# Kernel tuning notes

Hardware: AMD Instinct MI355X
Metric: run time of the kernel (lower is better)

## Reference

```python
import jax, jax.numpy as jnp
import numpy as np

K = 16          # neighbors per center (init arg K)
EPS = 1e-5      # layernorm epsilon


def _dcconv(pos, ch, W, b, n_in, n_out, resnet_in=None, Wres=None, bres=None):
    """KNN-gathered distance-contained conv.
    pos: [B, n_in, 3], ch: [B, n_in, Cin], W: [Cout, K, Cin].
    Selects n_out strided centers, gathers K nearest neighbors, convolves.
    """
    stride = n_in // n_out
    idx = jnp.arange(n_out) * stride                      # static center indices
    cpos = pos[:, idx]                                    # [B, n_out, 3]
    # squared pairwise distances centers -> all points: [B, n_out, n_in]
    d2 = jnp.sum((cpos[:, :, None, :] - pos[:, None, :, :]) ** 2, axis=-1)
    _, knn = jax.lax.top_k(-d2, K)                        # [B, n_out, K]
    gathered = jax.vmap(lambda c, i: c[i])(ch, knn)       # [B, n_out, K, Cin]
    out = jnp.einsum('bnkc,okc->bno', gathered, W) + b    # [B, n_out, Cout]
    if resnet_in is None:
        res = ch[:, idx] @ Wres + bres                    # project skip to Cout
    else:
        res = resnet_in[:, idx]                           # downsample carried skip
    return cpos, out, res


def _layernorm(x, g, b):
    mu = jnp.mean(x, axis=-1, keepdims=True)
    var = jnp.var(x, axis=-1, keepdims=True)
    return (x - mu) * jax.lax.rsqrt(var + EPS) * g + b


def setup_inputs() -> dict:
    key = jax.random.key(0)
    ks = jax.random.split(key, 8)
    B, N, Cin, Cout = 2, 8192, 64, 128
    s1 = (2.0 / (K * Cin)) ** 0.5
    s2 = (2.0 / (K * Cout)) ** 0.5
    return {
        'position_matrix': jax.random.normal(ks[0], (B, N, 3), jnp.float32),
        'channel_matrix': jax.random.normal(ks[1], (B, N, Cin), jnp.float32),
        'W1': jax.random.normal(ks[2], (Cout, K, Cin), jnp.float32) * s1,
        'b1': jnp.full((Cout,), 0.01, jnp.float32),
        'Wres': jax.random.normal(ks[3], (Cin, Cout), jnp.float32) * (2.0 / Cin) ** 0.5,
        'bres': jnp.full((Cout,), 0.01, jnp.float32),
        'W2': jax.random.normal(ks[4], (Cout, K, Cout), jnp.float32) * s2,
        'b2': jnp.full((Cout,), 0.01, jnp.float32),
        'g1': jnp.ones((Cout,), jnp.float32),
        'be1': jnp.full((Cout,), 0.01, jnp.float32),
        'g2': jnp.ones((Cout,), jnp.float32),
        'be2': jnp.full((Cout,), 0.01, jnp.float32),
        'n0': 8192, 'n1': 4096, 'n2': 2048,
    }


def reference(position_matrix, channel_matrix, W1, b1, Wres, bres, W2, b2,
              g1, be1, g2, be2, n0, n1, n2):
    pos, ch, res = _dcconv(position_matrix, channel_matrix, W1, b1, n0, n1,
                           None, Wres, bres)
    ch = jax.nn.silu(_layernorm(ch, g1, be1))   # dropout=identity (eval)
    pos, ch, res = _dcconv(pos, ch, W2, b2, n1, n2, resnet_in=res)
    ch = jax.nn.silu(_layernorm(ch, g2, be2))   # dropout=identity (eval)
    ch = ch + res                               # residual add
    return pos, ch
```

## Files before the change

### kernel.cpp

```cpp
#include <hip/hip_runtime.h>
#include <cstdint>
#include <cstddef>

using u16 = unsigned short;
using u32 = unsigned int;
using u64 = unsigned long long;

typedef short bf16x8 __attribute__((ext_vector_type(8)));
typedef float f32x4 __attribute__((ext_vector_type(4)));

constexpr int BATCH = 2;
constexpr int N0 = 8192;
constexpr int N1 = 4096;
constexpr int N2 = 2048;
constexpr int COUT = 128;
constexpr int KNB = 16;

__device__ __forceinline__ float bf2f(u16 v) { return __uint_as_float(((u32)v) << 16); }
__device__ __forceinline__ u16 f2bf(float f) {
    u32 u = __float_as_uint(f);
    return (u16)((u + 0x7fffu + ((u >> 16) & 1u)) >> 16);
}
__device__ __forceinline__ void cvt8(const float* __restrict__ src, u16* __restrict__ dst, int e) {
    float t0[8];
    *(float4*)t0 = *(const float4*)(src + e);
    *(float4*)(t0 + 4) = *(const float4*)(src + e + 4);
    u16 o[8];
#pragma unroll
    for (int q = 0; q < 8; ++q) o[q] = f2bf(t0[q]);
    *(uint4*)(dst + e) = *(uint4*)o;
}

__device__ __forceinline__ float dist2s(float cx, float cy, float cz,
                                        float px, float py, float pz) {
#pragma clang fp contract(off)
    float dx = cx - px;
    float dy = cy - py;
    float dz = cz - pz;
    float s = dx * dx;
    s = s + dy * dy;
    s = s + dz * dz;
    return s;
}

template <int CTRL>
__device__ __forceinline__ u64 dpp64(u64 v) {
    int lo = (int)(u32)v, hi = (int)(u32)(v >> 32);
    int plo = __builtin_amdgcn_update_dpp(0, lo, CTRL, 0xF, 0xF, true);
    int phi = __builtin_amdgcn_update_dpp(0, hi, CTRL, 0xF, 0xF, true);
    return (((u64)(u32)phi) << 32) | (u32)plo;
}
__device__ __forceinline__ u64 dpp_prev_u64(u64 v) { return dpp64<0x111>(v); }

__device__ __forceinline__ void knn_scan(const float* __restrict__ P, int pstride,
                                         int c0row, int c1row, int base, int cnt,
                                         int lane, u64& rk0, u64& rk1) {
    const float* c0p = P + (size_t)c0row * pstride;
    const float* c1p = P + (size_t)c1row * pstride;
    float c0x = c0p[0], c0y = c0p[1], c0z = c0p[2];
    float c1x = c1p[0], c1y = c1p[1], c1z = c1p[2];

    u64 key0, key1;
    {
        const float* pp = P + (size_t)(base + lane) * pstride;
        float px = pp[0], py = pp[1], pz = pp[2];
        u64 k0 = (((u64)__float_as_uint(dist2s(c0x, c0y, c0z, px, py, pz))) << 32) | (u32)(base + lane);
        u64 k1 = (((u64)__float_as_uint(dist2s(c1x, c1y, c1z, px, py, pz))) << 32) | (u32)(base + lane);
#pragma unroll
        for (int kk = 2; kk <= 64; kk <<= 1)
#pragma unroll
            for (int jj = kk >> 1; jj > 0; jj >>= 1) {
                u64 o0, o1;
                if (jj == 1)      { o0 = dpp64<0xB1>(k0);  o1 = dpp64<0xB1>(k1); }
                else if (jj == 2) { o0 = dpp64<0x4E>(k0);  o1 = dpp64<0x4E>(k1); }
                else if (jj == 8) { o0 = dpp64<0x128>(k0); o1 = dpp64<0x128>(k1); }
                else              { o0 = __shfl_xor(k0, jj, 64); o1 = __shfl_xor(k1, jj, 64); }
                bool keepmin = (((lane & jj) == 0) == ((lane & kk) == 0));
                k0 = keepmin ? ((o0 < k0) ? o0 : k0) : ((o0 > k0) ? o0 : k0);
                k1 = keepmin ? ((o1 < k1) ? o1 : k1) : ((o1 > k1) ? o1 : k1);
            }
        key0 = k0; key1 = k1;
    }
    u32 cut0 = __shfl((u32)(key0 >> 32), 15, 64);
    u32 cut1 = __shfl((u32)(key1 >> 32), 15, 64);

    int nstep = cnt >> 6;
    const float* pp = P + (size_t)(base + 64 + lane) * pstride;
    float pnx = pp[0], pny = pp[1], pnz = pp[2];
    for (int s = 1; s < nstep; ++s) {
        float px = pnx, py = pny, pz = pnz;
        int nx = (s + 1 < nstep) ? ((s + 1) << 6) : (s << 6);
        const float* np_ = P + (size_t)(base + nx + lane) * pstride;
        pnx = np_[0]; pny = np_[1]; pnz = np_[2];
        int sb = base + (s << 6);
        u32 d0 = __float_as_uint(dist2s(c0x, c0y, c0z, px, py, pz));
        u32 d1 = __float_as_uint(dist2s(c1x, c1y, c1z, px, py, pz));
        u64 ball0 = __ballot(d0 <= cut0);
        u64 ball1 = __ballot(d1 <= cut1);
        bool any0 = ball0 != 0, any1 = ball1 != 0;
        while (ball0 | ball1) {
            if (ball0) {
                int src = __ffsll((unsigned long long)ball0) - 1;
                ball0 &= ball0 - 1;
                u32 dn = __shfl(d0, src, 64);
                u64 nk = (((u64)dn) << 32) | (u32)(sb + src);
                u64 prev = dpp_prev_u64(key0);
                key0 = (nk < key0) ? ((nk < prev) ? prev : nk) : key0;
            }
            if (ball1) {
                int src = __ffsll((unsigned long long)ball1) - 1;
                ball1 &= ball1 - 1;
                u32 dn = __shfl(d1, src, 64);
                u64 nk = (((u64)dn) << 32) | (u32)(sb + src);
                u64 prev = dpp_prev_u64(key1);
                key1 = (nk < key1) ? ((nk < prev) ? prev : nk) : key1;
            }
        }
        if (any0) cut0 = __shfl((u32)(key0 >> 32), 15, 64);
        if (any1) cut1 = __shfl((u32)(key1 >> 32), 15, 64);
    }
    rk0 = key0; rk1 = key1;
}

__global__ __launch_bounds__(256)
void knn_prep_kernel(const float* __restrict__ pos0, const float* __restrict__ ch0,
                     const float* __restrict__ W1, const float* __restrict__ W2,
                     const float* __restrict__ Wres,
                     int* __restrict__ knn1, int* __restrict__ knn2,
                     u16* __restrict__ ch0b, u16* __restrict__ W1b,
                     u16* __restrict__ W2b, u16* __restrict__ Wresb,
                     float* __restrict__ pos_out) {
    int blk = blockIdx.x, tid = threadIdx.x;
    int w = tid >> 6, lane = tid & 63;
    if (blk < 1024) {
        int wave = blk * 4 + w;
        int batch = wave >> 11, pj = wave & 2047;
        const float* P = pos0 + (size_t)batch * N0 * 3;
        u64 key0, key1;
        knn_scan(P, 3, 4 * pj, 4 * pj + 2, 0, N0, lane, key0, key1);
        if (lane < 16) {
            knn1[((size_t)(batch * N1 + 2 * pj)) * KNB + lane] = (int)(u32)key0;
            knn1[((size_t)(batch * N1 + 2 * pj + 1)) * KNB + lane] = (int)(u32)key1;
        }
    } else if (blk < 1536) {
        int wave = (blk - 1024) * 4 + w;
        int batch = wave >> 10, pj = wave & 1023;
        const float* P = pos0 + (size_t)batch * N0 * 3;
        u64 key0, key1;
        knn_scan(P, 6, 4 * pj, 4 * pj + 2, 0, N1, lane, key0, key1);
        if (lane < 16) {
            knn2[((size_t)(batch * N2 + 2 * pj)) * KNB + lane] = (int)(u32)key0;
            knn2[((size_t)(batch * N2 + 2 * pj + 1)) * KNB + lane] = (int)(u32)key1;
        }
    } else if (blk < 2048) {
        cvt8(ch0, ch0b, ((blk - 1536) * 256 + tid) * 8);
    } else if (blk < 2112) {
        cvt8(W1, W1b, ((blk - 2048) * 256 + tid) * 8);
    } else if (blk < 2240) {
        cvt8(W2, W2b, ((blk - 2112) * 256 + tid) * 8);
    } else if (blk < 2272) {
        int t = (blk - 2240) * 256 + tid;
        int o = t >> 6, c = t & 63;
        Wresb[o * 64 + c] = f2bf(Wres[(size_t)c * COUT + o]);
    } else {
        int t = (blk - 2272) * 256 + tid;
        int b = t >> 11, r = t & 2047;
        const float* s = pos0 + ((size_t)(b * N0 + r * 4)) * 3;
        float* d = pos_out + ((size_t)(b * N2 + r)) * 3;
        d[0] = s[0]; d[1] = s[1]; d[2] = s[2];
    }
}

__global__ __launch_bounds__(256)
void conv1_kernel(const u16* __restrict__ ch0b, const int* __restrict__ knn1,
                  const u16* __restrict__ W1b, const u16* __restrict__ Wresb,
                  const float* __restrict__ b1, const float* __restrict__ bres,
                  const float* __restrict__ g1, const float* __restrict__ be1,
                  u16* __restrict__ ch1b, u16* __restrict__ res1b) {
    __shared__ u16 As[16][72];
    __shared__ u16 Ws[128][72];
    __shared__ int knnr[16][16];
    __shared__ float red[16][4][2];
    __shared__ float cb[128], cg[128], cbe[128], cbr[128];

    int tid = threadIdx.x;
    int blk = blockIdx.x;
    int b = blk >> 8, g = blk & 255;
    int jbase = g * 16;

    if (tid < 128) { cb[tid] = b1[tid]; cg[tid] = g1[tid]; cbe[tid] = be1[tid]; cbr[tid] = bres[tid]; }
    {
        int r = tid >> 4, k = tid & 15;
        knnr[r][k] = knn1[((size_t)(b * N1 + jbase + r)) * KNB + k];
    }
    __syncthreads();

    int w = tid >> 6, lane = tid & 63, quad = lane >> 4, l15 = lane & 15;
    int wcol = w * 32;
    int ar = tid >> 4, ap = tid & 15;
    int wn = tid >> 1, wh = tid & 1;

    f32x4 acc[2] = {{0,0,0,0},{0,0,0,0}};
    f32x4 racc[2] = {{0,0,0,0},{0,0,0,0}};

    uint2 aR = *((const uint2*)(ch0b + ((size_t)(b * N0 + knnr[ar][0])) * 64) + ap);
    uint4 wR[4];
    {
        const uint4* s4 = (const uint4*)(W1b + (size_t)wn * 1024 + wh * 32);
        wR[0] = s4[0]; wR[1] = s4[1]; wR[2] = s4[2]; wR[3] = s4[3];
    }
    for (int kn = 0; kn < 17; ++kn) {
        *(uint2*)&As[ar][ap * 4] = aR;
        uint4* d4 = (uint4*)&Ws[wn][wh * 32];
        d4[0] = wR[0]; d4[1] = wR[1]; d4[2] = wR[2]; d4[3] = wR[3];
        __syncthreads();
        if (kn < 16) {
            int nidx = (kn < 15) ? knnr[ar][kn + 1] : 2 * (jbase + ar);
            aR = *((const uint2*)(ch0b + ((size_t)(b * N0 + nidx)) * 64) + ap);
            const uint4* s4 = (kn < 15)
                ? (const uint4*)(W1b + (size_t)wn * 1024 + (kn + 1) * 64 + wh * 32)
                : (const uint4*)(Wresb + (size_t)wn * 64 + wh * 32);
            wR[0] = s4[0]; wR[1] = s4[1]; wR[2] = s4[2]; wR[3] = s4[3];
        }
        if (kn < 16) {
#pragma unroll
            for (int ks = 0; ks < 2; ++ks) {
                bf16x8 af = *(const bf16x8*)&As[l15][ks * 32 + quad * 8];
#pragma unroll
                for (int nt = 0; nt < 2; ++nt) {
                    bf16x8 bfr = *(const bf16x8*)&Ws[wcol + nt * 16 + l15][ks * 32 + quad * 8];
                    acc[nt] = __builtin_amdgcn_mfma_f32_16x16x32_bf16(af, bfr, acc[nt], 0, 0, 0);
                }
            }
        } else {
#pragma unroll
            for (int ks = 0; ks < 2; ++ks) {
                bf16x8 af = *(const bf16x8*)&As[l15][ks * 32 + quad * 8];
#pragma unroll
                for (int nt = 0; nt < 2; ++nt) {
                    bf16x8 bfr = *(const bf16x8*)&Ws[wcol + nt * 16 + l15][ks * 32 + quad * 8];
                    racc[nt] = __builtin_amdgcn_mfma_f32_16x16x32_bf16(af, bfr, racc[nt], 0, 0, 0);
                }
            }
        }
        __syncthreads();
    }

    float x[2][4], s[4] = {0,0,0,0}, ss[4] = {0,0,0,0};
#pragma unroll
    for (int reg = 0; reg < 4; ++reg)
#pragma unroll
        for (int nt = 0; nt < 2; ++nt) {
            int col = wcol + nt * 16 + l15;
            float v = acc[nt][reg] + cb[col];
            x[nt][reg] = v;
            s[reg] += v; ss[reg] += v * v;
        }
#pragma unroll
    for (int m = 1; m < 16; m <<= 1)
#pragma unroll
        for (int reg = 0; reg < 4; ++reg) {
            s[reg] += __shfl_xor(s[reg], m, 64);
            ss[reg] += __shfl_xor(ss[reg], m, 64);
        }
    if (l15 == 0) {
#pragma unroll
        for (int reg = 0; reg < 4; ++reg) {
            red[quad * 4 + reg][w][0] = s[reg];
            red[quad * 4 + reg][w][1] = ss[reg];
        }
    }
    __syncthreads();
    float mu[4], rs[4];
#pragma unroll
    for (int reg = 0; reg < 4; ++reg) {
        int row = quad * 4 + reg;
        float S = red[row][0][0] + red[row][1][0] + red[row][2][0] + red[row][3][0];
        float SS = red[row][0][1] + red[row][1][1] + red[row][2][1] + red[row][3][1];
        mu[reg] = S * (1.f / 128.f);
        float var = fmaxf(SS * (1.f / 128.f) - mu[reg] * mu[reg], 0.f);
        rs[reg] = 1.f / sqrtf(var + 1e-5f);
    }
#pragma unroll
    for (int nt = 0; nt < 2; ++nt)
#pragma unroll
        for (int reg = 0; reg < 4; ++reg) {
            int col = wcol + nt * 16 + l15;
            int row = quad * 4 + reg;
            size_t off = ((size_t)(b * N1 + jbase + row)) * COUT + col;
            float y = (x[nt][reg] - mu[reg]) * rs[reg] * cg[col] + cbe[col];
            ch1b[off] = f2bf(y / (1.f + __expf(-y)));
            res1b[off] = f2bf(racc[nt][reg] + cbr[col]);
        }
}

__global__ __launch_bounds__(512)
void conv2_kernel(const u16* __restrict__ ch1b, const int* __restrict__ knn2,
                  const u16* __restrict__ W2b, const float* __restrict__ b2,
                  const float* __restrict__ g2, const float* __restrict__ be2,
                  const u16* __restrict__ res1b, float* __restrict__ ch_out) {
    __shared__ u16 As[16][136];
    __shared__ u16 Ws[128][136];
    __shared__ int knnr[16][16];
    __shared__ float red[16][8][2];
    __shared__ float cb[128], cg[128], cbe[128];

    int tid = threadIdx.x;
    int b = blockIdx.x >> 7, g = blockIdx.x & 127;
    int ibase = g * 16;

    if (tid < 128) { cb[tid] = b2[tid]; cg[tid] = g2[tid]; cbe[tid] = be2[tid]; }
    if (tid < 256) {
        int r = tid >> 4, k = tid & 15;
        knnr[r][k] = knn2[((size_t)(b * N2 + ibase + r)) * KNB + k];
    }
    __syncthreads();

    int w = tid >> 6, lane = tid & 63, quad = lane >> 4, l15 = lane & 15;
    int wcol = w * 16;
    int ar = tid >> 5, ap = tid & 31;
    int wn = tid >> 2, wq = tid & 3;

    f32x4 acc = {0, 0, 0, 0};

    uint2 aR = *((const uint2*)(ch1b + ((size_t)(b * N1 + knnr[ar][0])) * COUT) + ap);
    uint4 wR[4];
    {
        const uint4* s4 = (const uint4*)(W2b + (size_t)wn * 2048 + wq * 32);
        wR[0] = s4[0]; wR[1] = s4[1]; wR[2] = s4[2]; wR[3] = s4[3];
    }
    for (int kn = 0; kn < 16; ++kn) {
        *(uint2*)&As[ar][ap * 4] = aR;
        uint4* d4 = (uint4*)&Ws[wn][wq * 32];
        d4[0] = wR[0]; d4[1] = wR[1]; d4[2] = wR[2]; d4[3] = wR[3];
        __syncthreads();
        if (kn < 15) {
            aR = *((const uint2*)(ch1b + ((size_t)(b * N1 + knnr[ar][kn + 1])) * COUT) + ap);
            const uint4* s4 = (const uint4*)(W2b + (size_t)wn * 2048 + (kn + 1) * 128 + wq * 32);
            wR[0] = s4[0]; wR[1] = s4[1]; wR[2] = s4[2]; wR[3] = s4[3];
        }
#pragma unroll
        for (int ks = 0; ks < 4; ++ks) {
            bf16x8 af = *(const bf16x8*)&As[l15][ks * 32 + quad * 8];
            bf16x8 bfr = *(const bf16x8*)&Ws[wcol + l15][ks * 32 + quad * 8];
            acc = __builtin_amdgcn_mfma_f32_16x16x32_bf16(af, bfr, acc, 0, 0, 0);
        }
        __syncthreads();
    }

    float x[4], s[4], ss[4];
#pragma unroll
    for (int reg = 0; reg < 4; ++reg) {
        int col = wcol + l15;
        float v = acc[reg] + cb[col];
        x[reg] = v; s[reg] = v; ss[reg] = v * v;
    }
#pragma unroll
    for (int m = 1; m < 16; m <<= 1)
#pragma unroll
        for (int reg = 0; reg < 4; ++reg) {
            s[reg] += __shfl_xor(s[reg], m, 64);
            ss[reg] += __shfl_xor(ss[reg], m, 64);
        }
    if (l15 == 0) {
#pragma unroll
        for (int reg = 0; reg < 4; ++reg) {
            red[quad * 4 + reg][w][0] = s[reg];
            red[quad * 4 + reg][w][1] = ss[reg];
        }
    }
    __syncthreads();
#pragma unroll
    for (int reg = 0; reg < 4; ++reg) {
        int row = quad * 4 + reg;
        float S = 0.f, SS = 0.f;
#pragma unroll
        for (int t = 0; t < 8; ++t) { S += red[row][t][0]; SS += red[row][t][1]; }
        float mu = S * (1.f / 128.f);
        float var = fmaxf(SS * (1.f / 128.f) - mu * mu, 0.f);
        float rs = 1.f / sqrtf(var + 1e-5f);
        int col = wcol + l15;
        int i = ibase + row;
        float y = (x[reg] - mu) * rs * cg[col] + cbe[col];
        float sl = y / (1.f + __expf(-y));
        float rv = bf2f(res1b[((size_t)(b * N1 + 2 * i)) * COUT + col]);
        ch_out[((size_t)(b * N2 + i)) * COUT + col] = sl + rv;
    }
}

extern "C" void kernel_launch(void* const* d_in, const int* in_sizes, int n_in,
                              void* d_out, int out_size, void* d_ws, size_t ws_size,
                              hipStream_t stream) {
    const float* pos0 = (const float*)d_in[0];
    const float* ch0  = (const float*)d_in[1];
    const float* W1   = (const float*)d_in[2];
    const float* b1   = (const float*)d_in[3];
    const float* Wres = (const float*)d_in[4];
    const float* bres = (const float*)d_in[5];
    const float* W2   = (const float*)d_in[6];
    const float* b2   = (const float*)d_in[7];
    const float* g1   = (const float*)d_in[8];
    const float* be1  = (const float*)d_in[9];
    const float* g2   = (const float*)d_in[10];
    const float* be2  = (const float*)d_in[11];
    float* out = (float*)d_out;

    char* ws = (char*)d_ws;
    int*  knn1  = (int*)(ws);
    int*  knn2  = (int*)(ws + 524288);
    u16*  ch0b  = (u16*)(ws + 786432);
    u16*  W1b   = (u16*)(ws + 2883584);
    u16*  W2b   = (u16*)(ws + 3145728);
    u16*  Wresb = (u16*)(ws + 3670016);
    u16*  ch1b  = (u16*)(ws + 3686400);
    u16*  res1b = (u16*)(ws + 5783552);

    float* pos_out = out;
    float* ch_out  = out + 12288;

    knn_prep_kernel<<<2288, 256, 0, stream>>>(pos0, ch0, W1, W2, Wres,
                                              knn1, knn2, ch0b, W1b, W2b, Wresb, pos_out);
    conv1_kernel<<<512, 256, 0, stream>>>(ch0b, knn1, W1b, Wresb, b1, bres, g1, be1, ch1b, res1b);
    conv2_kernel<<<256, 512, 0, stream>>>(ch1b, knn2, W2b, b2, g2, be2, res1b, ch_out);
}
```

Before: 224.5 us.

## Split stage-1 KNN scan across two waves and merge with bitonic sort

Result: slower. 242.2 us (+7.9%).

```diff
diff --git a/kernel.cpp b/kernel.cpp
--- a/kernel.cpp
+++ b/kernel.cpp
@@ -130,20 +130,38 @@
                      u16* __restrict__ ch0b, u16* __restrict__ W1b,
                      u16* __restrict__ W2b, u16* __restrict__ Wresb,
                      float* __restrict__ pos_out) {
+    __shared__ u64 mk[2][2][2][16];
     int blk = blockIdx.x, tid = threadIdx.x;
     int w = tid >> 6, lane = tid & 63;
-    if (blk < 1024) {
-        int wave = blk * 4 + w;
-        int batch = wave >> 11, pj = wave & 2047;
+    if (blk < 2048) {
+        int pi = w >> 1, h = w & 1;
+        int p = blk * 2 + pi;
+        int batch = p >> 11, pj = p & 2047;
         const float* P = pos0 + (size_t)batch * N0 * 3;
         u64 key0, key1;
-        knn_scan(P, 3, 4 * pj, 4 * pj + 2, 0, N0, lane, key0, key1);
-        if (lane < 16) {
-            knn1[((size_t)(batch * N1 + 2 * pj)) * KNB + lane] = (int)(u32)key0;
-            knn1[((size_t)(batch * N1 + 2 * pj + 1)) * KNB + lane] = (int)(u32)key1;
-        }
-    } else if (blk < 1536) {
-        int wave = (blk - 1024) * 4 + w;
+        knn_scan(P, 3, 4 * pj, 4 * pj + 2, h * 4096, 4096, lane, key0, key1);
+        if (lane < 16) { mk[pi][h][0][lane] = key0; mk[pi][h][1][lane] = key1; }
+        __syncthreads();
+        if (h == 0) {
+            int c = lane >> 5, l = lane & 31;
+            u64 k = mk[pi][l >> 4][c][l & 15];
+#pragma unroll
+            for (int kk = 2; kk <= 32; kk <<= 1)
+#pragma unroll
+                for (int jj = kk >> 1; jj > 0; jj >>= 1) {
+                    u64 o;
+                    if (jj == 1)      o = dpp64<0xB1>(k);
+                    else if (jj == 2) o = dpp64<0x4E>(k);
+                    else if (jj == 8) o = dpp64<0x128>(k);
+                    else              o = __shfl_xor(k, jj, 64);
+                    bool keepmin = (((l & jj) == 0) == ((l & kk) == 0));
+                    k = keepmin ? ((o < k) ? o : k) : ((o > k) ? o : k);
+                }
+            if (l < 16)
+                knn1[((size_t)(batch * N1 + 2 * pj + c)) * KNB + l] = (int)(u32)k;
+        }
+    } else if (blk < 2560) {
+        int wave = (blk - 2048) * 4 + w;
         int batch = wave >> 10, pj = wave & 1023;
         const float* P = pos0 + (size_t)batch * N0 * 3;
         u64 key0, key1;
@@ -152,18 +170,18 @@
             knn2[((size_t)(batch * N2 + 2 * pj)) * KNB + lane] = (int)(u32)key0;
             knn2[((size_t)(batch * N2 + 2 * pj + 1)) * KNB + lane] = (int)(u32)key1;
         }
-    } else if (blk < 2048) {
-        cvt8(ch0, ch0b, ((blk - 1536) * 256 + tid) * 8);
-    } else if (blk < 2112) {
-        cvt8(W1, W1b, ((blk - 2048) * 256 + tid) * 8);
-    } else if (blk < 2240) {
-        cvt8(W2, W2b, ((blk - 2112) * 256 + tid) * 8);
-    } else if (blk < 2272) {
-        int t = (blk - 2240) * 256 + tid;
+    } else if (blk < 3072) {
+        cvt8(ch0, ch0b, ((blk - 2560) * 256 + tid) * 8);
+    } else if (blk < 3136) {
+        cvt8(W1, W1b, ((blk - 3072) * 256 + tid) * 8);
+    } else if (blk < 3264) {
+        cvt8(W2, W2b, ((blk - 3136) * 256 + tid) * 8);
+    } else if (blk < 3296) {
+        int t = (blk - 3264) * 256 + tid;
         int o = t >> 6, c = t & 63;
         Wresb[o * 64 + c] = f2bf(Wres[(size_t)c * COUT + o]);
     } else {
-        int t = (blk - 2272) * 256 + tid;
+        int t = (blk - 3296) * 256 + tid;
         int b = t >> 11, r = t & 2047;
         const float* s = pos0 + ((size_t)(b * N0 + r * 4)) * 3;
         float* d = pos_out + ((size_t)(b * N2 + r)) * 3;
@@ -418,7 +436,7 @@
     float* pos_out = out;
     float* ch_out  = out + 12288;
 
-    knn_prep_kernel<<<2288, 256, 0, stream>>>(pos0, ch0, W1, W2, Wres,
+    knn_prep_kernel<<<3312, 256, 0, stream>>>(pos0, ch0, W1, W2, Wres,
                                               knn1, knn2, ch0b, W1b, W2b, Wresb, pos_out);
     conv1_kernel<<<512, 256, 0, stream>>>(ch0b, knn1, W1b, Wresb, b1, bres, g1, be1, ch1b, res1b);
     conv2_kernel<<<256, 512, 0, stream>>>(ch1b, knn2, W2b, b2, g2, be2, res1b, ch_out);
```
